# Performance work log

Hardware: AMD Instinct MI355X
Metric: run time of the kernel (lower is better)

The kernel has to match this reference:

```python
import jax, jax.numpy as jnp
import numpy as np

EPS = 1e-6
NH, HD = 8, 16            # num_heads, head_dim (dim=128)
KSS, DILS, HPR = (3, 5), (1, 2), (6, 2)  # kernel sizes, dilations, heads per range (favor_small)


def gelu(t):
    return jax.nn.gelu(t, approximate=False)


def conv1x1(x, w, b):
    # x: (B,C,H,W), w: (O,C), b: (O,)
    return jnp.einsum('oc,bchw->bohw', w, x) + b[None, :, None, None]


def dwconv(x, w, b, dil=1):
    # depthwise conv, w: (C,1,k,k)
    k = w.shape[-1]
    p = (k // 2) * dil
    y = jax.lax.conv_general_dilated(
        x, w, window_strides=(1, 1), padding=[(p, p), (p, p)],
        rhs_dilation=(dil, dil), feature_group_count=x.shape[1],
        dimension_numbers=('NCHW', 'OIHW', 'NCHW'))
    return y + b[None, :, None, None]


def ln2d(x, w, b):
    # LayerNorm over channel dim of NCHW
    mu = x.mean(axis=1, keepdims=True)
    var = ((x - mu) ** 2).mean(axis=1, keepdims=True)
    return (x - mu) * jax.lax.rsqrt(var + EPS) * w[None, :, None, None] + b[None, :, None, None]


def unfold(x, ks, dil):
    # x: (B,h,d,H,W) -> (B,h,d,L,H,W) with L=ks*ks neighborhood (row-major, matches F.unfold)
    B, h, d, H, W = x.shape
    p = (ks // 2) * dil
    xp = jnp.pad(x, ((0, 0), (0, 0), (0, 0), (p, p), (p, p)))
    patches = [xp[..., i * dil:i * dil + H, j * dil:j * dil + W]
               for i in range(ks) for j in range(ks)]
    return jnp.stack(patches, axis=3)


def neighborhood_attn(x, qkv_ws, qkv_bs, proj_w, proj_b):
    B, C, H, W = x.shape
    scale = HD ** -0.5
    outs, hs = [], 0
    for i in range(2):
        qkv = conv1x1(x, qkv_ws[i], qkv_bs[i]).reshape(B, 3, NH, HD, H, W)
        he = hs + HPR[i]
        q, k, v = qkv[:, 0, hs:he], qkv[:, 1, hs:he], qkv[:, 2, hs:he]
        k_nb = unfold(k, KSS[i], DILS[i])  # (B,h,d,L,H,W)
        v_nb = unfold(v, KSS[i], DILS[i])
        logits = jnp.einsum('bhdxy,bhdlxy->bhlxy', q * scale, k_nb)
        attn = jax.nn.softmax(logits, axis=2)
        outs.append(jnp.einsum('bhlxy,bhdlxy->bhdxy', attn, v_nb))
        hs = he
    out = jnp.concatenate(outs, axis=1).reshape(B, C, H, W)
    return conv1x1(out, proj_w, proj_b)


def msconvstar(x, fc1_w, fc1_b, dw_ws, dw_bs, fc2_w, fc2_b):
    h = conv1x1(x, fc1_w, fc1_b)                  # (B,192,H,W)
    xs = jnp.split(h, [64, 128], axis=1)          # channels [64,64,64] for dw_sizes (1,3,5)
    ys = [dwconv(t, w, b) for t, w, b in zip(xs, dw_ws, dw_bs)]
    h = h + jnp.concatenate(ys, axis=1)
    x1, x2 = jnp.split(h, 2, axis=1)
    return conv1x1(gelu(x1) * x2, fc2_w, fc2_b)


def cascaded_sparse(x, dw0_w, dw0_b, dw1_w, dw1_b, pw_w, pw_b):
    x = gelu(dwconv(x, dw0_w, dw0_b, dil=1))
    x = gelu(dwconv(x, dw1_w, dw1_b, dil=2))
    return conv1x1(x, pw_w, pw_b)


def setup_inputs() -> dict:
    key = jax.random.key(0)
    ks = jax.random.split(key, 24)
    C, HID = 128, 192

    def p(k, shape, s=0.02):
        return jax.random.normal(k, shape, jnp.float32) * s

    d = {'x': jax.random.normal(ks[0], (4, C, 80, 80), jnp.float32)}
    for i in (1, 2, 3, 4):
        d[f'n{i}_w'] = jnp.ones((C,), jnp.float32)
        d[f'n{i}_b'] = jnp.zeros((C,), jnp.float32)
    d['qkv0_w'] = p(ks[1], (3 * C, C)); d['qkv0_b'] = jnp.zeros((3 * C,), jnp.float32)
    d['qkv1_w'] = p(ks[2], (3 * C, C)); d['qkv1_b'] = jnp.zeros((3 * C,), jnp.float32)
    d['ma_proj_w'] = p(ks[3], (C, C)); d['ma_proj_b'] = jnp.zeros((C,), jnp.float32)
    for pre, k0 in (('m1', 4), ('m2', 10)):
        d[f'{pre}_fc1_w'] = p(ks[k0], (HID, C)); d[f'{pre}_fc1_b'] = jnp.zeros((HID,), jnp.float32)
        for j, dk in enumerate((1, 3, 5)):
            d[f'{pre}_dw{j}_w'] = p(ks[k0 + 1 + j], (64, 1, dk, dk))
            d[f'{pre}_dw{j}_b'] = jnp.zeros((64,), jnp.float32)
        d[f'{pre}_fc2_w'] = p(ks[k0 + 4], (C, HID // 2)); d[f'{pre}_fc2_b'] = jnp.zeros((C,), jnp.float32)
    d['sma_dw0_w'] = p(ks[16], (C, 1, 3, 3)); d['sma_dw0_b'] = jnp.zeros((C,), jnp.float32)
    d['sma_dw1_w'] = p(ks[17], (C, 1, 3, 3)); d['sma_dw1_b'] = jnp.zeros((C,), jnp.float32)
    d['sma_pw_w'] = p(ks[18], (C, C)); d['sma_pw_b'] = jnp.zeros((C,), jnp.float32)
    return d


def reference(x, n1_w, n1_b, n2_w, n2_b, n3_w, n3_b, n4_w, n4_b,
              qkv0_w, qkv0_b, qkv1_w, qkv1_b, ma_proj_w, ma_proj_b,
              m1_fc1_w, m1_fc1_b, m1_dw0_w, m1_dw0_b, m1_dw1_w, m1_dw1_b,
              m1_dw2_w, m1_dw2_b, m1_fc2_w, m1_fc2_b,
              sma_dw0_w, sma_dw0_b, sma_dw1_w, sma_dw1_b, sma_pw_w, sma_pw_b,
              m2_fc1_w, m2_fc1_b, m2_dw0_w, m2_dw0_b, m2_dw1_w, m2_dw1_b,
              m2_dw2_w, m2_dw2_b, m2_fc2_w, m2_fc2_b):
    x = x + neighborhood_attn(ln2d(x, n1_w, n1_b), (qkv0_w, qkv1_w), (qkv0_b, qkv1_b), ma_proj_w, ma_proj_b)
    x = x + msconvstar(ln2d(x, n2_w, n2_b), m1_fc1_w, m1_fc1_b,
                       (m1_dw0_w, m1_dw1_w, m1_dw2_w), (m1_dw0_b, m1_dw1_b, m1_dw2_b), m1_fc2_w, m1_fc2_b)
    x = x + cascaded_sparse(ln2d(x, n3_w, n3_b), sma_dw0_w, sma_dw0_b, sma_dw1_w, sma_dw1_b, sma_pw_w, sma_pw_b)
    x = x + msconvstar(ln2d(x, n4_w, n4_b), m2_fc1_w, m2_fc1_b,
                       (m2_dw0_w, m2_dw1_w, m2_dw2_w), (m2_dw0_b, m2_dw1_b, m2_dw2_b), m2_fc2_w, m2_fc2_b)
    return x
```

## Files before the change

### kernel.cpp

```cpp
#include <hip/hip_runtime.h>
#include <math.h>

#define Hn 80
#define Wn 80
#define HWn 6400

typedef unsigned short u16;
typedef __attribute__((ext_vector_type(8))) short s16x8;
typedef __attribute__((ext_vector_type(4))) float f32x4;

__device__ __forceinline__ float gelu_exact(float v) {
  return 0.5f * v * (1.f + erff(v * 0.70710678118654752f));
}
__device__ __forceinline__ u16 f2bf(float x) {
  unsigned u = __float_as_uint(x);
  return (u16)((u + 0x7fffu + ((u >> 16) & 1u)) >> 16);
}
__device__ __forceinline__ float bf2f(u16 h) {
  return __uint_as_float(((unsigned)h) << 16);
}
typedef __attribute__((address_space(1))) const unsigned int* gptr_t;
typedef __attribute__((address_space(3))) unsigned int* lptr_t;
__device__ __forceinline__ void gld16(const void* g, void* l) {
  __builtin_amdgcn_global_load_lds((gptr_t)g, (lptr_t)l, 16, 0, 0);
}
__device__ __forceinline__ void ld16h(const u16* p, float* f) {
  uint4 a = *(const uint4*)p;
  uint4 c = *(const uint4*)(p + 8);
  unsigned w[8] = {a.x, a.y, a.z, a.w, c.x, c.y, c.z, c.w};
  #pragma unroll
  for (int j = 0; j < 8; ++j) {
    f[2 * j]     = __uint_as_float(w[j] << 16);
    f[2 * j + 1] = __uint_as_float(w[j] & 0xffff0000u);
  }
}

__global__ __launch_bounds__(256) void wprep_k(
    const float* __restrict__ q0w, const float* __restrict__ q0b,
    const float* __restrict__ q1w, const float* __restrict__ q1b,
    const float* __restrict__ projw, const float* __restrict__ f1w_1,
    const float* __restrict__ f2w_1, const float* __restrict__ pww,
    const float* __restrict__ f1w_2, const float* __restrict__ f2w_2,
    u16* Wq, float* Bq, u16* Wp, u16* Wf1a, u16* Wf2a, u16* Wpw, u16* Wf1b, u16* Wf2b) {
  int idx = blockIdx.x * 256 + threadIdx.x;
  if (idx < 49152) {
    int r = idx >> 7, ic = idx & 127;
    int sel = r >> 7, c = r & 127;
    const float* src = ((c >> 4) < 6 ? q0w : q1w);
    Wq[idx] = f2bf(src[(size_t)(sel * 128 + c) * 128 + ic]);
    return;
  }
  idx -= 49152;
  if (idx < 16384) { Wp[idx] = f2bf(projw[idx]); return; }
  idx -= 16384;
  if (idx < 24576) { Wf1a[idx] = f2bf(f1w_1[idx]); return; }
  idx -= 24576;
  if (idx < 16384) { int oc = idx >> 7, ic = idx & 127;
    Wf2a[idx] = ic < 96 ? f2bf(f2w_1[oc * 96 + ic]) : (u16)0; return; }
  idx -= 16384;
  if (idx < 16384) { Wpw[idx] = f2bf(pww[idx]); return; }
  idx -= 16384;
  if (idx < 24576) { Wf1b[idx] = f2bf(f1w_2[idx]); return; }
  idx -= 24576;
  if (idx < 16384) { int oc = idx >> 7, ic = idx & 127;
    Wf2b[idx] = ic < 96 ? f2bf(f2w_2[oc * 96 + ic]) : (u16)0; return; }
  idx -= 16384;
  if (idx < 384) {
    int sel = idx >> 7, c = idx & 127;
    Bq[idx] = ((c >> 4) < 6 ? q0b : q1b)[sel * 128 + c];
  }
}

__global__ __launch_bounds__(256) void ln_k(const float* __restrict__ in,
    const float* __restrict__ gw, const float* __restrict__ gb, u16* __restrict__ outv) {
  __shared__ float sS[4][64];
  __shared__ float sQ[4][64];
  __shared__ unsigned sT[64 * 64];
  const int b = blockIdx.y;
  const int p0 = blockIdx.x * 64;
  const int tid = threadIdx.x;
  const int px = tid & 63;
  const int cg = tid >> 6;
  const float* ip = in + (size_t)b * 128 * HWn + p0 + px;
  float s = 0.f, q = 0.f;
  #pragma unroll 8
  for (int c = cg * 32; c < cg * 32 + 32; ++c) { float v = ip[(size_t)c * HWn]; s += v; q += v * v; }
  sS[cg][px] = s; sQ[cg][px] = q;
  __syncthreads();
  float S = sS[0][px] + sS[1][px] + sS[2][px] + sS[3][px];
  float Q = sQ[0][px] + sQ[1][px] + sQ[2][px] + sQ[3][px];
  float mu = S * (1.f / 128.f);
  float rs = rsqrtf(Q * (1.f / 128.f) - mu * mu + 1e-6f);
  #pragma unroll
  for (int j = 0; j < 16; ++j) {
    int c0 = cg * 32 + 2 * j;
    float v0 = ip[(size_t)c0 * HWn];
    float v1 = ip[(size_t)(c0 + 1) * HWn];
    v0 = (v0 - mu) * rs * gw[c0] + gb[c0];
    v1 = (v1 - mu) * rs * gw[c0 + 1] + gb[c0 + 1];
    int wc = cg * 16 + j;
    sT[px * 64 + (wc ^ (px & 31))] = (unsigned)f2bf(v0) | ((unsigned)f2bf(v1) << 16);
  }
  __syncthreads();
  u16* ob = outv + ((size_t)b * HWn + p0) * 128;
  #pragma unroll
  for (int it = 0; it < 4; ++it) {
    int opx = it * 16 + (tid >> 4);
    int chunk = tid & 15;
    unsigned w[4];
    #pragma unroll
    for (int j = 0; j < 4; ++j)
      w[j] = sT[opx * 64 + ((chunk * 4 + j) ^ (opx & 31))];
    *(uint4*)(ob + (size_t)opx * 128 + chunk * 8) = make_uint4(w[0], w[1], w[2], w[3]);
  }
}

__global__ __launch_bounds__(256) void lnstats_k(const float* __restrict__ in,
                                                 float2* __restrict__ st) {
  __shared__ float sS[4][64];
  __shared__ float sQ[4][64];
  const int b = blockIdx.y;
  const int p0 = blockIdx.x * 64;
  const int tid = threadIdx.x;
  const int px = tid & 63;
  const int cg = tid >> 6;
  const float* ip = in + (size_t)b * 128 * HWn + p0 + px;
  float s = 0.f, q = 0.f;
  #pragma unroll 8
  for (int c = cg * 32; c < cg * 32 + 32; ++c) { float v = ip[(size_t)c * HWn]; s += v; q += v * v; }
  sS[cg][px] = s; sQ[cg][px] = q;
  __syncthreads();
  if (cg == 0) {
    float S = sS[0][px] + sS[1][px] + sS[2][px] + sS[3][px];
    float Q = sQ[0][px] + sQ[1][px] + sQ[2][px] + sQ[3][px];
    float mu = S * (1.f / 128.f);
    float rs = rsqrtf(Q * (1.f / 128.f) - mu * mu + 1e-6f);
    st[(size_t)b * HWn + p0 + px] = make_float2(mu, rs);
  }
}

__device__ __forceinline__ s16x8 ldfrag(const u16* s, int row, int gk) {
  return *(const s16x8*)(s + row * 128 + ((gk ^ (row & 7)) << 3));
}

template<int ORIENT, int RES, int SPLITQ, int H16>
__global__ __launch_bounds__(256) void gemm_k(
    const u16* __restrict__ Xg, const u16* __restrict__ Wg,
    const float* __restrict__ bias, const float* __restrict__ resid,
    float* __restrict__ outF, u16* __restrict__ outH, int OCT) {
  __shared__ u16 sX[128 * 128];
  __shared__ u16 sW[64 * 128];
  const int tid = threadIdx.x, lane = tid & 63, wv = tid >> 6;
  const int b = blockIdx.y;
  const int px0 = blockIdx.x * 128;
  const int oc0 = blockIdx.z * 64;
  const u16* xb = Xg + ((size_t)b * HWn + px0) * 128;
  const u16* wb = Wg + (size_t)oc0 * 128;
  #pragma unroll
  for (int i = 0; i < 8; ++i) {
    int o16 = (wv * 8 + i) * 64 + lane;
    int r = o16 >> 4, g = o16 & 15;
    gld16(xb + (size_t)r * 128 + ((g ^ (r & 7)) << 3), (char*)sX + (size_t)(wv * 8 + i) * 1024);
  }
  #pragma unroll
  for (int i = 0; i < 4; ++i) {
    int o16 = (wv * 4 + i) * 64 + lane;
    int r = o16 >> 4, g = o16 & 15;
    gld16(wb + (size_t)r * 128 + ((g ^ (r & 7)) << 3), (char*)sW + (size_t)(wv * 4 + i) * 1024);
  }
  __syncthreads();
  const int l15 = lane & 15, l4 = lane >> 4;
  if (ORIENT == 0) {
    f32x4 acc[4][2] = {};
    #pragma unroll
    for (int ks = 0; ks < 4; ++ks) {
      int gk = ks * 4 + l4;
      s16x8 a[4], bb[2];
      #pragma unroll
      for (int mi = 0; mi < 4; ++mi) a[mi] = ldfrag(sW, mi * 16 + l15, gk);
      #pragma unroll
      for (int ni = 0; ni < 2; ++ni) bb[ni] = ldfrag(sX, wv * 32 + ni * 16 + l15, gk);
      #pragma unroll
      for (int mi = 0; mi < 4; ++mi)
        #pragma unroll
        for (int ni = 0; ni < 2; ++ni)
          acc[mi][ni] = __builtin_amdgcn_mfma_f32_16x16x32_bf16(a[mi], bb[ni], acc[mi][ni], 0, 0, 0);
    }
    #pragma unroll
    for (int mi = 0; mi < 4; ++mi) {
      #pragma unroll
      for (int rr = 0; rr < 4; ++rr) {
        int oc = oc0 + mi * 16 + l4 * 4 + rr;
        float bv = bias[oc];
        #pragma unroll
        for (int ni = 0; ni < 2; ++ni) {
          size_t idx = ((size_t)b * OCT + oc) * HWn + px0 + wv * 32 + ni * 16 + l15;
          float v = acc[mi][ni][rr] + bv;
          if (H16) {
            outH[idx] = f2bf(v);
          } else {
            if (RES) v += resid[idx];
            outF[idx] = v;
          }
        }
      }
    }
  } else {
    f32x4 acc[2][4] = {};
    #pragma unroll
    for (int ks = 0; ks < 4; ++ks) {
      int gk = ks * 4 + l4;
      s16x8 a[2], bb[4];
      #pragma unroll
      for (int mi = 0; mi < 2; ++mi) a[mi] = ldfrag(sX, wv * 32 + mi * 16 + l15, gk);
      #pragma unroll
      for (int ni = 0; ni < 4; ++ni) bb[ni] = ldfrag(sW, ni * 16 + l15, gk);
      #pragma unroll
      for (int mi = 0; mi < 2; ++mi)
        #pragma unroll
        for (int ni = 0; ni < 4; ++ni)
          acc[mi][ni] = __builtin_amdgcn_mfma_f32_16x16x32_bf16(a[mi], bb[ni], acc[mi][ni], 0, 0, 0);
    }
    #pragma unroll
    for (int ni = 0; ni < 4; ++ni) {
      int oc = oc0 + ni * 16 + l15;
      float bv = bias[oc];
      #pragma unroll
      for (int mi = 0; mi < 2; ++mi) {
        #pragma unroll
        for (int rr = 0; rr < 4; ++rr) {
          int px = px0 + wv * 32 + mi * 16 + l4 * 4 + rr;
          float v = acc[mi][ni][rr] + bv;
          u16 hv = f2bf(v);
          if (SPLITQ) {
            int sel = oc >> 7, c = oc & 127;
            int head = c >> 4, d = c & 15;
            outH[((((size_t)sel * 8 + head) * 4 + b) * HWn + px) * 16 + d] = hv;
          } else {
            outH[((size_t)b * HWn + px) * (size_t)OCT + oc] = hv;
          }
        }
      }
    }
  }
}

template<int KS, int DIL>
__global__ __launch_bounds__(256) void natt_k(const u16* __restrict__ qkv,
                                              u16* __restrict__ out, int h0) {
  constexpr int HALO = DIL * (KS / 2);
  constexpr int D = 16 + 2 * HALO;
  __shared__ u16 sK[D * D * 16];
  __shared__ u16 sV[D * D * 16];
  const int b = blockIdx.y, h = h0 + blockIdx.z;
  const int tile = blockIdx.x;
  const int ty0 = (tile / 5) * 16, tx0 = (tile % 5) * 16;
  const int tid = threadIdx.x;
  const int ly = tid >> 4, lx = tid & 15;
  const u16* Qb = qkv + (((size_t)h * 4 + b) * HWn) * 16;
  const u16* Kb = qkv + ((((size_t)8 + h) * 4 + b) * HWn) * 16;
  const u16* Vb = qkv + ((((size_t)16 + h) * 4 + b) * HWn) * 16;
  for (int i = tid; i < D * D * 2; i += 256) {
    int pxi = i >> 1, half = i & 1;
    int ey = pxi / D, ex = pxi - ey * D;
    int gy = ty0 - HALO + ey, gx = tx0 - HALO + ex;
    uint4 kv = make_uint4(0, 0, 0, 0), vv = make_uint4(0, 0, 0, 0);
    if (gy >= 0 && gy < Hn && gx >= 0 && gx < Wn) {
      size_t off = (size_t)(gy * Wn + gx) * 16 + half * 8;
      kv = *(const uint4*)(Kb + off);
      vv = *(const uint4*)(Vb + off);
    }
    *(uint4*)(sK + pxi * 16 + half * 8) = kv;
    *(uint4*)(sV + pxi * 16 + half * 8) = vv;
  }
  const int p = (ty0 + ly) * Wn + tx0 + lx;
  float qv[16];
  ld16h(Qb + (size_t)p * 16, qv);
  #pragma unroll
  for (int d = 0; d < 16; ++d) qv[d] *= 0.25f;
  __syncthreads();
  constexpr int L = KS * KS;
  float lg[L];
  #pragma unroll
  for (int i = 0; i < KS; ++i) {
    #pragma unroll
    for (int j = 0; j < KS; ++j) {
      float kvv[16];
      ld16h(sK + (size_t)((ly + i * DIL) * D + lx + j * DIL) * 16, kvv);
      float a = 0.f;
      #pragma unroll
      for (int d = 0; d < 16; ++d) a = fmaf(qv[d], kvv[d], a);
      lg[i * KS + j] = a;
    }
  }
  float mx = lg[0];
  #pragma unroll
  for (int l = 1; l < L; ++l) mx = fmaxf(mx, lg[l]);
  float sum = 0.f;
  #pragma unroll
  for (int l = 0; l < L; ++l) { float e = __expf(lg[l] - mx); lg[l] = e; sum += e; }
  float inv = 1.f / sum;
  float acc[16];
  #pragma unroll
  for (int d = 0; d < 16; ++d) acc[d] = 0.f;
  #pragma unroll
  for (int i = 0; i < KS; ++i) {
    #pragma unroll
    for (int j = 0; j < KS; ++j) {
      float vv[16];
      ld16h(sV + (size_t)((ly + i * DIL) * D + lx + j * DIL) * 16, vv);
      float wl = lg[i * KS + j] * inv;
      #pragma unroll
      for (int d = 0; d < 16; ++d) acc[d] = fmaf(wl, vv[d], acc[d]);
    }
  }
  unsigned wst[8];
  #pragma unroll
  for (int j = 0; j < 8; ++j)
    wst[j] = (unsigned)f2bf(acc[2 * j]) | ((unsigned)f2bf(acc[2 * j + 1]) << 16);
  u16* op = out + ((size_t)b * HWn + p) * 128 + h * 16;
  *(uint4*)op = make_uint4(wst[0], wst[1], wst[2], wst[3]);
  *(uint4*)(op + 8) = make_uint4(wst[4], wst[5], wst[6], wst[7]);
}

template<int R>
__device__ __forceinline__ void stage_plane(const u16* __restrict__ plane,
                                            float* __restrict__ s,
                                            int ty0, int tx0, int tid) {
  constexpr int D = 16 + 2 * R, PD = D + 1;
  #pragma unroll
  for (int i = tid; i < D * D; i += 256) {
    int ey = i / D, ex = i - ey * D;
    int gy = ty0 - R + ey, gx = tx0 - R + ex;
    float v = 0.f;
    if (gy >= 0 && gy < Hn && gx >= 0 && gx < Wn) v = bf2f(plane[gy * Wn + gx]);
    s[ey * PD + ex] = v;
  }
}

template<int R>
__device__ __forceinline__ float dw_from_lds(const float* __restrict__ s, int ly, int lx,
                                             const float* __restrict__ w, float bv) {
  constexpr int PD = 16 + 2 * R + 1;
  float center = s[(ly + R) * PD + (lx + R)];
  float acc = bv;
  #pragma unroll
  for (int i = 0; i < 2 * R + 1; ++i)
    #pragma unroll
    for (int j = 0; j < 2 * R + 1; ++j)
      acc = fmaf(w[i * (2 * R + 1) + j], s[(ly + i) * PD + (lx + j)], acc);
  return center + acc;
}

template<int R1, int R2>
__device__ __forceinline__ void star_pairs(const u16* __restrict__ hb,
    const float* __restrict__ w0, const float* __restrict__ b0,
    const float* __restrict__ w1, const float* __restrict__ b1,
    const float* __restrict__ w2, const float* __restrict__ b2,
    float* __restrict__ s1_0, float* __restrict__ s1_1,
    float* __restrict__ s2_0, float* __restrict__ s2_1,
    int z, int ty0, int tx0, int tid, int ly, int lx, unsigned* __restrict__ res) {
  if (R1 > 0) stage_plane<R1>(hb + (size_t)(z * 8) * HWn, s1_0, ty0, tx0, tid);
  stage_plane<R2>(hb + (size_t)(z * 8 + 96) * HWn, s2_0, ty0, tx0, tid);
  __syncthreads();
  #pragma unroll 1
  for (int pi = 0; pi < 8; ++pi) {
    int c1 = z * 8 + pi;
    int c2 = c1 + 96;
    float* s1c = (pi & 1) ? s1_1 : s1_0;
    float* s2c = (pi & 1) ? s2_1 : s2_0;
    if (pi < 7) {
      float* s1n = (pi & 1) ? s1_0 : s1_1;
      float* s2n = (pi & 1) ? s2_0 : s2_1;
      if (R1 > 0) stage_plane<R1>(hb + (size_t)(c1 + 1) * HWn, s1n, ty0, tx0, tid);
      stage_plane<R2>(hb + (size_t)(c2 + 1) * HWn, s2n, ty0, tx0, tid);
    }
    float h1;
    if constexpr (R1 == 0) {
      float cen = bf2f(hb[(size_t)c1 * HWn + (ty0 + ly) * Wn + tx0 + lx]);
      h1 = cen + fmaf(cen, w0[c1], b0[c1]);
    } else {
      h1 = dw_from_lds<R1>(s1c, ly, lx, w1 + (c1 - 64) * 9, b1[c1 - 64]);
    }
    float h2;
    if constexpr (R2 == 1) {
      h2 = dw_from_lds<1>(s2c, ly, lx, w1 + (c2 - 64) * 9, b1[c2 - 64]);
    } else {
      h2 = dw_from_lds<2>(s2c, ly, lx, w2 + (c2 - 128) * 25, b2[c2 - 128]);
    }
    u16 gv = f2bf(gelu_exact(h1) * h2);
    if (pi & 1) res[pi >> 1] |= ((unsigned)gv) << 16;
    else        res[pi >> 1] = (unsigned)gv;
    __syncthreads();
  }
}

__global__ __launch_bounds__(256) void star_k(const u16* __restrict__ hbuf,
    const float* __restrict__ w0, const float* __restrict__ b0,
    const float* __restrict__ w1, const float* __restrict__ b1,
    const float* __restrict__ w2, const float* __restrict__ b2,
    u16* __restrict__ g) {
  __shared__ float s1_0[18 * 19];
  __shared__ float s1_1[18 * 19];
  __shared__ float s2_0[20 * 21];
  __shared__ float s2_1[20 * 21];
  const int b = blockIdx.y, z = blockIdx.z;
  const int tile = blockIdx.x;
  const int ty0 = (tile / 5) * 16, tx0 = (tile % 5) * 16;
  const int tid = threadIdx.x;
  const int ly = tid >> 4, lx = tid & 15;
  const u16* hb = hbuf + (size_t)b * 192 * HWn;
  unsigned res[4];
  if (z < 4)      star_pairs<0, 1>(hb, w0, b0, w1, b1, w2, b2, s1_0, s1_1, s2_0, s2_1, z, ty0, tx0, tid, ly, lx, res);
  else if (z < 8) star_pairs<0, 2>(hb, w0, b0, w1, b1, w2, b2, s1_0, s1_1, s2_0, s2_1, z, ty0, tx0, tid, ly, lx, res);
  else            star_pairs<1, 2>(hb, w0, b0, w1, b1, w2, b2, s1_0, s1_1, s2_0, s2_1, z, ty0, tx0, tid, ly, lx, res);
  const int px = (ty0 + ly) * Wn + tx0 + lx;
  *(uint4*)(g + ((size_t)b * HWn + px) * 128 + z * 8) = make_uint4(res[0], res[1], res[2], res[3]);
  if (z < 4)
    *(uint4*)(g + ((size_t)b * HWn + px) * 128 + 96 + z * 8) = make_uint4(0, 0, 0, 0);
}

__global__ __launch_bounds__(256) void dwgf_k(const float* __restrict__ xin,
    const float2* __restrict__ st,
    const float* __restrict__ gw, const float* __restrict__ gb,
    const float* __restrict__ w1, const float* __restrict__ b1,
    const float* __restrict__ w2, const float* __restrict__ b2,
    u16* __restrict__ out) {
  __shared__ float sA[22 * 23];
  __shared__ float sB[20 * 21];
  __shared__ float sMu[22 * 22];
  __shared__ float sRs[22 * 22];
  const int b = blockIdx.y, z = blockIdx.z;
  const int tile = blockIdx.x;
  const int ty0 = (tile / 5) * 16, tx0 = (tile % 5) * 16;
  const int tid = threadIdx.x;
  const int ly = tid >> 4, lx = tid & 15;
  #pragma unroll
  for (int i = tid; i < 22 * 22; i += 256) {
    int ey = i / 22, ex = i - ey * 22;
    int gy = ty0 - 3 + ey, gx = tx0 - 3 + ex;
    float2 s = make_float2(0.f, 0.f);
    if (gy >= 0 && gy < Hn && gx >= 0 && gx < Wn) s = st[(size_t)b * HWn + gy * Wn + gx];
    sMu[i] = s.x; sRs[i] = s.y;
  }
  const float* xb = xin + (size_t)b * 128 * HWn;
  unsigned res[4];
  #pragma unroll 1
  for (int ci = 0; ci < 8; ++ci) {
    int c = z * 8 + ci;
    const float* xp = xb + (size_t)c * HWn;
    float gwc = gw[c], gbc = gb[c];
    __syncthreads();
    #pragma unroll
    for (int i = tid; i < 22 * 22; i += 256) {
      int ey = i / 22, ex = i - ey * 22;
      int gy = ty0 - 3 + ey, gx = tx0 - 3 + ex;
      float v = 0.f;
      if (gy >= 0 && gy < Hn && gx >= 0 && gx < Wn)
        v = (xp[gy * Wn + gx] - sMu[i]) * sRs[i] * gwc + gbc;
      sA[ey * 23 + ex] = v;
    }
    __syncthreads();
    #pragma unroll
    for (int j = tid; j < 20 * 20; j += 256) {
      int by = j / 20, bx = j - by * 20;
      int gy = ty0 - 2 + by, gx = tx0 - 2 + bx;
      float r = 0.f;
      if (gy >= 0 && gy < Hn && gx >= 0 && gx < Wn) {
        float acc = b1[c];
        #pragma unroll
        for (int di = 0; di < 3; ++di)
          #pragma unroll
          for (int dj = 0; dj < 3; ++dj)
            acc = fmaf(w1[c * 9 + di * 3 + dj], sA[(by + di) * 23 + (bx + dj)], acc);
        r = gelu_exact(acc);
      }
      sB[by * 21 + bx] = r;
    }
    __syncthreads();
    float acc = b2[c];
    #pragma unroll
    for (int di = 0; di < 3; ++di)
      #pragma unroll
      for (int dj = 0; dj < 3; ++dj)
        acc = fmaf(w2[c * 9 + di * 3 + dj], sB[(ly + 2 * di) * 21 + (lx + 2 * dj)], acc);
    float r = gelu_exact(acc);
    u16 gv = f2bf(r);
    if (ci & 1) res[ci >> 1] |= ((unsigned)gv) << 16;
    else        res[ci >> 1] = (unsigned)gv;
  }
  const int px = (ty0 + ly) * Wn + tx0 + lx;
  *(uint4*)(out + ((size_t)b * HWn + px) * 128 + z * 8) = make_uint4(res[0], res[1], res[2], res[3]);
}

extern "C" void kernel_launch(void* const* d_in, const int* in_sizes, int n_in,
                              void* d_out, int out_size, void* d_ws, size_t ws_size,
                              hipStream_t stream) {
  (void)in_sizes; (void)n_in; (void)out_size; (void)ws_size;
  const float* x      = (const float*)d_in[0];
  const float* n1w    = (const float*)d_in[1];
  const float* n1b    = (const float*)d_in[2];
  const float* n2w    = (const float*)d_in[3];
  const float* n2b    = (const float*)d_in[4];
  const float* n3w    = (const float*)d_in[5];
  const float* n3b    = (const float*)d_in[6];
  const float* n4w    = (const float*)d_in[7];
  const float* n4b    = (const float*)d_in[8];
  const float* qkv0w  = (const float*)d_in[9];
  const float* qkv0b  = (const float*)d_in[10];
  const float* qkv1w  = (const float*)d_in[11];
  const float* qkv1b  = (const float*)d_in[12];
  const float* projw  = (const float*)d_in[13];
  const float* projb  = (const float*)d_in[14];
  const float* m1fc1w = (const float*)d_in[15];
  const float* m1fc1b = (const float*)d_in[16];
  const float* m1dw0w = (const float*)d_in[17];
  const float* m1dw0b = (const float*)d_in[18];
  const float* m1dw1w = (const float*)d_in[19];
  const float* m1dw1b = (const float*)d_in[20];
  const float* m1dw2w = (const float*)d_in[21];
  const float* m1dw2b = (const float*)d_in[22];
  const float* m1fc2w = (const float*)d_in[23];
  const float* m1fc2b = (const float*)d_in[24];
  const float* smadw0w = (const float*)d_in[25];
  const float* smadw0b = (const float*)d_in[26];
  const float* smadw1w = (const float*)d_in[27];
  const float* smadw1b = (const float*)d_in[28];
  const float* smapww  = (const float*)d_in[29];
  const float* smapwb  = (const float*)d_in[30];
  const float* m2fc1w = (const float*)d_in[31];
  const float* m2fc1b = (const float*)d_in[32];
  const float* m2dw0w = (const float*)d_in[33];
  const float* m2dw0b = (const float*)d_in[34];
  const float* m2dw1w = (const float*)d_in[35];
  const float* m2dw1b = (const float*)d_in[36];
  const float* m2dw2w = (const float*)d_in[37];
  const float* m2dw2b = (const float*)d_in[38];
  const float* m2fc2w = (const float*)d_in[39];
  const float* m2fc2b = (const float*)d_in[40];

  float* out = (float*)d_out;
  char* wsb = (char*)d_ws;
  u16*  QKV = (u16*)(wsb + 0);
  u16*  Hb16 = (u16*)(wsb + 0);
  u16*  LNo = (u16*)(wsb + 19660800);
  u16*  ATT = (u16*)(wsb + 26214400);
  u16*  T2  = (u16*)(wsb + 32768000);
  char* wp = wsb + 39321600;
  u16* Wq    = (u16*)wp;  wp += 98304;
  u16* Wproj = (u16*)wp;  wp += 32768;
  u16* Wf1a  = (u16*)wp;  wp += 49152;
  u16* Wf2a  = (u16*)wp;  wp += 32768;
  u16* Wpw   = (u16*)wp;  wp += 32768;
  u16* Wf1b  = (u16*)wp;  wp += 49152;
  u16* Wf2b  = (u16*)wp;  wp += 32768;
  float* Bq  = (float*)wp; wp += 2048;
  float2* Stats = (float2*)wp;

  dim3 blk(256);
  wprep_k<<<642, blk, 0, stream>>>(qkv0w, qkv0b, qkv1w, qkv1b, projw, m1fc1w, m1fc2w,
                                   smapww, m2fc1w, m2fc2w,
                                   Wq, Bq, Wproj, Wf1a, Wf2a, Wpw, Wf1b, Wf2b);

  ln_k<<<dim3(100, 4), blk, 0, stream>>>(x, n1w, n1b, LNo);
  gemm_k<1, 0, 1, 0><<<dim3(50, 4, 6), blk, 0, stream>>>(LNo, Wq, Bq, nullptr, nullptr, QKV, 384);
  natt_k<3, 1><<<dim3(25, 4, 6), blk, 0, stream>>>(QKV, ATT, 0);
  natt_k<5, 2><<<dim3(25, 4, 2), blk, 0, stream>>>(QKV, ATT, 6);
  gemm_k<0, 1, 0, 0><<<dim3(50, 4, 2), blk, 0, stream>>>(ATT, Wproj, projb, x, out, nullptr, 128);

  ln_k<<<dim3(100, 4), blk, 0, stream>>>(out, n2w, n2b, LNo);
  gemm_k<0, 0, 0, 1><<<dim3(50, 4, 3), blk, 0, stream>>>(LNo, Wf1a, m1fc1b, nullptr, nullptr, Hb16, 192);
  star_k<<<dim3(25, 4, 12), blk, 0, stream>>>(Hb16, m1dw0w, m1dw0b, m1dw1w, m1dw1b, m1dw2w, m1dw2b, ATT);
  gemm_k<0, 1, 0, 0><<<dim3(50, 4, 2), blk, 0, stream>>>(ATT, Wf2a, m1fc2b, out, out, nullptr, 128);

  lnstats_k<<<dim3(100, 4), blk, 0, stream>>>(out, Stats);
  dwgf_k<<<dim3(25, 4, 16), blk, 0, stream>>>(out, Stats, n3w, n3b,
                                              smadw0w, smadw0b, smadw1w, smadw1b, T2);
  gemm_k<0, 1, 0, 0><<<dim3(50, 4, 2), blk, 0, stream>>>(T2, Wpw, smapwb, out, out, nullptr, 128);

  ln_k<<<dim3(100, 4), blk, 0, stream>>>(out, n4w, n4b, LNo);
  gemm_k<0, 0, 0, 1><<<dim3(50, 4, 3), blk, 0, stream>>>(LNo, Wf1b, m2fc1b, nullptr, nullptr, Hb16, 192);
  star_k<<<dim3(25, 4, 12), blk, 0, stream>>>(Hb16, m2dw0w, m2dw0b, m2dw1w, m2dw1b, m2dw2w, m2dw2b, ATT);
  gemm_k<0, 1, 0, 0><<<dim3(50, 4, 2), blk, 0, stream>>>(ATT, Wf2b, m2fc2b, out, out, nullptr, 128);
}
```

Baseline: 163.9 us.

## Fuse residual GEMMs with following LayerNorm and merge neighborhood attention launches

```diff
diff --git a/kernel.cpp b/kernel.cpp
--- a/kernel.cpp
+++ b/kernel.cpp
@@ -115,39 +115,14 @@
   }
 }
 
-__global__ __launch_bounds__(256) void lnstats_k(const float* __restrict__ in,
-                                                 float2* __restrict__ st) {
-  __shared__ float sS[4][64];
-  __shared__ float sQ[4][64];
-  const int b = blockIdx.y;
-  const int p0 = blockIdx.x * 64;
-  const int tid = threadIdx.x;
-  const int px = tid & 63;
-  const int cg = tid >> 6;
-  const float* ip = in + (size_t)b * 128 * HWn + p0 + px;
-  float s = 0.f, q = 0.f;
-  #pragma unroll 8
-  for (int c = cg * 32; c < cg * 32 + 32; ++c) { float v = ip[(size_t)c * HWn]; s += v; q += v * v; }
-  sS[cg][px] = s; sQ[cg][px] = q;
-  __syncthreads();
-  if (cg == 0) {
-    float S = sS[0][px] + sS[1][px] + sS[2][px] + sS[3][px];
-    float Q = sQ[0][px] + sQ[1][px] + sQ[2][px] + sQ[3][px];
-    float mu = S * (1.f / 128.f);
-    float rs = rsqrtf(Q * (1.f / 128.f) - mu * mu + 1e-6f);
-    st[(size_t)b * HWn + p0 + px] = make_float2(mu, rs);
-  }
-}
-
 __device__ __forceinline__ s16x8 ldfrag(const u16* s, int row, int gk) {
   return *(const s16x8*)(s + row * 128 + ((gk ^ (row & 7)) << 3));
 }
 
-template<int ORIENT, int RES, int SPLITQ, int H16>
+template<int ORIENT, int SPLITQ, int H16>
 __global__ __launch_bounds__(256) void gemm_k(
     const u16* __restrict__ Xg, const u16* __restrict__ Wg,
-    const float* __restrict__ bias, const float* __restrict__ resid,
-    float* __restrict__ outF, u16* __restrict__ outH, int OCT) {
+    const float* __restrict__ bias, u16* __restrict__ outH, int OCT) {
   __shared__ u16 sX[128 * 128];
   __shared__ u16 sW[64 * 128];
   const int tid = threadIdx.x, lane = tid & 63, wv = tid >> 6;
@@ -195,13 +170,7 @@
         #pragma unroll
         for (int ni = 0; ni < 2; ++ni) {
           size_t idx = ((size_t)b * OCT + oc) * HWn + px0 + wv * 32 + ni * 16 + l15;
-          float v = acc[mi][ni][rr] + bv;
-          if (H16) {
-            outH[idx] = f2bf(v);
-          } else {
-            if (RES) v += resid[idx];
-            outF[idx] = v;
-          }
+          outH[idx] = f2bf(acc[mi][ni][rr] + bv);
         }
       }
     }
@@ -232,31 +201,101 @@
           int px = px0 + wv * 32 + mi * 16 + l4 * 4 + rr;
           float v = acc[mi][ni][rr] + bv;
           u16 hv = f2bf(v);
-          if (SPLITQ) {
-            int sel = oc >> 7, c = oc & 127;
-            int head = c >> 4, d = c & 15;
-            outH[((((size_t)sel * 8 + head) * 4 + b) * HWn + px) * 16 + d] = hv;
-          } else {
-            outH[((size_t)b * HWn + px) * (size_t)OCT + oc] = hv;
-          }
+          int sel = oc >> 7, c = oc & 127;
+          int head = c >> 4, d = c & 15;
+          outH[((((size_t)sel * 8 + head) * 4 + b) * HWn + px) * 16 + d] = hv;
         }
       }
     }
   }
 }
 
+template<int EPI>
+__global__ __launch_bounds__(256) void gemm64_k(
+    const u16* __restrict__ Xg, const u16* __restrict__ Wg,
+    const float* __restrict__ bias, const float* __restrict__ resid,
+    float* __restrict__ outF, u16* __restrict__ outLN, float2* __restrict__ stats,
+    const float* __restrict__ gw, const float* __restrict__ gb) {
+  __shared__ u16 sX[64 * 128];
+  __shared__ u16 sW[128 * 128];
+  const int tid = threadIdx.x, lane = tid & 63, wv = tid >> 6;
+  const int b = blockIdx.y;
+  const int px0 = blockIdx.x * 64;
+  const u16* xb = Xg + ((size_t)b * HWn + px0) * 128;
+  #pragma unroll
+  for (int i = 0; i < 4; ++i) {
+    int o16 = (wv * 4 + i) * 64 + lane;
+    int r = o16 >> 4, g = o16 & 15;
+    gld16(xb + (size_t)r * 128 + ((g ^ (r & 7)) << 3), (char*)sX + (size_t)(wv * 4 + i) * 1024);
+  }
+  #pragma unroll
+  for (int i = 0; i < 8; ++i) {
+    int o16 = (wv * 8 + i) * 64 + lane;
+    int r = o16 >> 4, g = o16 & 15;
+    gld16(Wg + (size_t)r * 128 + ((g ^ (r & 7)) << 3), (char*)sW + (size_t)(wv * 8 + i) * 1024);
+  }
+  __syncthreads();
+  const int l15 = lane & 15, l4 = lane >> 4;
+  f32x4 acc[8] = {};
+  #pragma unroll
+  for (int ks = 0; ks < 4; ++ks) {
+    int gk = ks * 4 + l4;
+    s16x8 bb = ldfrag(sX, wv * 16 + l15, gk);
+    #pragma unroll
+    for (int mi = 0; mi < 8; ++mi) {
+      s16x8 a = ldfrag(sW, mi * 16 + l15, gk);
+      acc[mi] = __builtin_amdgcn_mfma_f32_16x16x32_bf16(a, bb, acc[mi], 0, 0, 0);
+    }
+  }
+  const int pxg = px0 + wv * 16 + l15;
+  float v[8][4];
+  float s = 0.f, q = 0.f;
+  #pragma unroll
+  for (int mi = 0; mi < 8; ++mi) {
+    #pragma unroll
+    for (int rr = 0; rr < 4; ++rr) {
+      int oc = mi * 16 + l4 * 4 + rr;
+      float t = acc[mi][rr] + bias[oc];
+      t += resid[((size_t)b * 128 + oc) * HWn + pxg];
+      v[mi][rr] = t;
+      s += t;
+      q = fmaf(t, t, q);
+    }
+  }
+  #pragma unroll
+  for (int mi = 0; mi < 8; ++mi)
+    #pragma unroll
+    for (int rr = 0; rr < 4; ++rr) {
+      int oc = mi * 16 + l4 * 4 + rr;
+      outF[((size_t)b * 128 + oc) * HWn + pxg] = v[mi][rr];
+    }
+  if (EPI == 0) return;
+  s += __shfl_xor(s, 16); s += __shfl_xor(s, 32);
+  q += __shfl_xor(q, 16); q += __shfl_xor(q, 32);
+  float mu = s * (1.f / 128.f);
+  float rs = rsqrtf(q * (1.f / 128.f) - mu * mu + 1e-6f);
+  if (EPI == 1) {
+    u16* lp = outLN + ((size_t)b * HWn + pxg) * 128;
+    #pragma unroll
+    for (int mi = 0; mi < 8; ++mi) {
+      int oc0 = mi * 16 + l4 * 4;
+      unsigned lo = (unsigned)f2bf((v[mi][0] - mu) * rs * gw[oc0] + gb[oc0])
+                  | ((unsigned)f2bf((v[mi][1] - mu) * rs * gw[oc0 + 1] + gb[oc0 + 1]) << 16);
+      unsigned hi = (unsigned)f2bf((v[mi][2] - mu) * rs * gw[oc0 + 2] + gb[oc0 + 2])
+                  | ((unsigned)f2bf((v[mi][3] - mu) * rs * gw[oc0 + 3] + gb[oc0 + 3]) << 16);
+      *(uint2*)(lp + oc0) = make_uint2(lo, hi);
+    }
+  } else {
+    if (l4 == 0) stats[(size_t)b * HWn + pxg] = make_float2(mu, rs);
+  }
+}
+
 template<int KS, int DIL>
-__global__ __launch_bounds__(256) void natt_k(const u16* __restrict__ qkv,
-                                              u16* __restrict__ out, int h0) {
+__device__ __forceinline__ void natt_body(const u16* __restrict__ qkv,
+    u16* __restrict__ out, u16* __restrict__ sK, u16* __restrict__ sV,
+    int b, int h, int ty0, int tx0, int tid, int ly, int lx) {
   constexpr int HALO = DIL * (KS / 2);
   constexpr int D = 16 + 2 * HALO;
-  __shared__ u16 sK[D * D * 16];
-  __shared__ u16 sV[D * D * 16];
-  const int b = blockIdx.y, h = h0 + blockIdx.z;
-  const int tile = blockIdx.x;
-  const int ty0 = (tile / 5) * 16, tx0 = (tile % 5) * 16;
-  const int tid = threadIdx.x;
-  const int ly = tid >> 4, lx = tid & 15;
   const u16* Qb = qkv + (((size_t)h * 4 + b) * HWn) * 16;
   const u16* Kb = qkv + ((((size_t)8 + h) * 4 + b) * HWn) * 16;
   const u16* Vb = qkv + ((((size_t)16 + h) * 4 + b) * HWn) * 16;
@@ -321,6 +360,19 @@
   u16* op = out + ((size_t)b * HWn + p) * 128 + h * 16;
   *(uint4*)op = make_uint4(wst[0], wst[1], wst[2], wst[3]);
   *(uint4*)(op + 8) = make_uint4(wst[4], wst[5], wst[6], wst[7]);
+}
+
+__global__ __launch_bounds__(256) void natt_k(const u16* __restrict__ qkv,
+                                              u16* __restrict__ out) {
+  __shared__ u16 sK[24 * 24 * 16];
+  __shared__ u16 sV[24 * 24 * 16];
+  const int b = blockIdx.y, h = blockIdx.z;
+  const int tile = blockIdx.x;
+  const int ty0 = (tile / 5) * 16, tx0 = (tile % 5) * 16;
+  const int tid = threadIdx.x;
+  const int ly = tid >> 4, lx = tid & 15;
+  if (h < 6) natt_body<3, 1>(qkv, out, sK, sV, b, h, ty0, tx0, tid, ly, lx);
+  else       natt_body<5, 2>(qkv, out, sK, sV, b, h, ty0, tx0, tid, ly, lx);
 }
 
 template<int R>
@@ -563,23 +615,19 @@
                                    Wq, Bq, Wproj, Wf1a, Wf2a, Wpw, Wf1b, Wf2b);
 
   ln_k<<<dim3(100, 4), blk, 0, stream>>>(x, n1w, n1b, LNo);
-  gemm_k<1, 0, 1, 0><<<dim3(50, 4, 6), blk, 0, stream>>>(LNo, Wq, Bq, nullptr, nullptr, QKV, 384);
-  natt_k<3, 1><<<dim3(25, 4, 6), blk, 0, stream>>>(QKV, ATT, 0);
-  natt_k<5, 2><<<dim3(25, 4, 2), blk, 0, stream>>>(QKV, ATT, 6);
-  gemm_k<0, 1, 0, 0><<<dim3(50, 4, 2), blk, 0, stream>>>(ATT, Wproj, projb, x, out, nullptr, 128);
-
-  ln_k<<<dim3(100, 4), blk, 0, stream>>>(out, n2w, n2b, LNo);
-  gemm_k<0, 0, 0, 1><<<dim3(50, 4, 3), blk, 0, stream>>>(LNo, Wf1a, m1fc1b, nullptr, nullptr, Hb16, 192);
+  gemm_k<1, 1, 0><<<dim3(50, 4, 6), blk, 0, stream>>>(LNo, Wq, Bq, QKV, 384);
+  natt_k<<<dim3(25, 4, 8), blk, 0, stream>>>(QKV, ATT);
+  gemm64_k<1><<<dim3(100, 4), blk, 0, stream>>>(ATT, Wproj, projb, x, out, LNo, nullptr, n2w, n2b);
+
+  gemm_k<0, 0, 1><<<dim3(50, 4, 3), blk, 0, stream>>>(LNo, Wf1a, m1fc1b, Hb16, 192);
   star_k<<<dim3(25, 4, 12), blk, 0, stream>>>(Hb16, m1dw0w, m1dw0b, m1dw1w, m1dw1b, m1dw2w, m1dw2b, ATT);
-  gemm_k<0, 1, 0, 0><<<dim3(50, 4, 2), blk, 0, stream>>>(ATT, Wf2a, m1fc2b, out, out, nullptr, 128);
-
-  lnstats_k<<<dim3(100, 4), blk, 0, stream>>>(out, Stats);
+  gemm64_k<2><<<dim3(100, 4), blk, 0, stream>>>(ATT, Wf2a, m1fc2b, out, out, nullptr, Stats, nullptr, nullptr);
+
   dwgf_k<<<dim3(25, 4, 16), blk, 0, stream>>>(out, Stats, n3w, n3b,
                                               smadw0w, smadw0b, smadw1w, smadw1b, T2);
-  gemm_k<0, 1, 0, 0><<<dim3(50, 4, 2), blk, 0, stream>>>(T2, Wpw, smapwb, out, out, nullptr, 128);
-
-  ln_k<<<dim3(100, 4), blk, 0, stream>>>(out, n4w, n4b, LNo);
-  gemm_k<0, 0, 0, 1><<<dim3(50, 4, 3), blk, 0, stream>>>(LNo, Wf1b, m2fc1b, nullptr, nullptr, Hb16, 192);
+  gemm64_k<1><<<dim3(100, 4), blk, 0, stream>>>(T2, Wpw, smapwb, out, out, LNo, nullptr, n4w, n4b);
+
+  gemm_k<0, 0, 1><<<dim3(50, 4, 3), blk, 0, stream>>>(LNo, Wf1b, m2fc1b, Hb16, 192);
   star_k<<<dim3(25, 4, 12), blk, 0, stream>>>(Hb16, m2dw0w, m2dw0b, m2dw1w, m2dw1b, m2dw2w, m2dw2b, ATT);
-  gemm_k<0, 1, 0, 0><<<dim3(50, 4, 2), blk, 0, stream>>>(ATT, Wf2b, m2fc2b, out, out, nullptr, 128);
-}
+  gemm64_k<0><<<dim3(100, 4), blk, 0, stream>>>(ATT, Wf2b, m2fc2b, out, out, nullptr, nullptr, nullptr, nullptr);
+}
```

After: 166.3 us. No clear change (+1.5%).
